# Kernel optimization log

Hardware: AMD Instinct MI355X
Metric: run time of the kernel (lower is better)

The kernel has to match this reference:

```python
import jax, jax.numpy as jnp
import numpy as np

B, T, C, H = 4, 4096, 1024, 64


def setup_inputs() -> dict:
    key = jax.random.key(0)
    k1, k2, k3, k4 = jax.random.split(key, 4)
    x = jax.random.normal(k1, (B, T, C), dtype=jnp.float32)
    # nn.Linear(C, H, bias=False) weights, stored as [C, H] so y = x @ W
    Wq = jax.random.normal(k2, (C, H), dtype=jnp.float32) * (C ** -0.5)
    Wk = jax.random.normal(k3, (C, H), dtype=jnp.float32) * (C ** -0.5)
    Wv = jax.random.normal(k4, (C, H), dtype=jnp.float32) * (C ** -0.5)
    return {"x": x, "Wq": Wq, "Wk": Wk, "Wv": Wv}


def reference(x, Wq, Wk, Wv):
    # x: (B,T,C) -> q,k,v: (B,T,H)
    q = jnp.einsum('btc,ch->bth', x, Wq)
    k = jnp.einsum('btc,ch->bth', x, Wk)
    v = jnp.einsum('btc,ch->bth', x, Wv)
    scale = q.shape[-1] ** -0.5
    # (B,T,T) attention scores with causal mask
    scores = jnp.einsum('bqh,bkh->bqk', q, k) * scale
    t = x.shape[1]
    causal = jnp.tril(jnp.ones((t, t), dtype=bool))
    scores = jnp.where(causal, scores, -jnp.inf)
    attn = jax.nn.softmax(scores, axis=-1)
    return jnp.einsum('bqk,bkh->bqh', attn, v)
```

## Files before the change

kernel.cpp:

```cpp
#include <hip/hip_runtime.h>

#define BATCH 4
#define SEQ   4096
#define CDIM  1024
#define HDIM  64

typedef __attribute__((ext_vector_type(8))) short bf16x8;
typedef __attribute__((ext_vector_type(4))) float f32x4;

#define WT_OFF 0
#define Q_OFF  (3 * HDIM * CDIM)
#define KF_OFF (Q_OFF + BATCH * SEQ * HDIM)
#define VF_OFF (KF_OFF + BATCH * SEQ * HDIM)

static __device__ __forceinline__ short f2bf(float f) {
  union { float f; unsigned u; } a; a.f = f;
  unsigned r = a.u + 0x7fffu + ((a.u >> 16) & 1u);
  return (short)(r >> 16);
}

static __device__ __forceinline__ bf16x8 ld8(const short* p) {
  return *(const bf16x8*)p;
}

__global__ void wcvt_kernel(const float* __restrict__ wq, const float* __restrict__ wk,
                            const float* __restrict__ wv, short* __restrict__ wt2) {
  int idx = blockIdx.x * 256 + threadIdx.x;
  int m = idx >> 16;
  int f = idx & 65535;
  int k0g = f >> 11, hc = (f >> 9) & 3, lr = (f >> 5) & 15, lg = (f >> 3) & 3, j = f & 7;
  int c = k0g * 32 + lg * 8 + j, h = hc * 16 + lr;
  const float* w = (m == 0) ? wq : (m == 1) ? wk : wv;
  wt2[((k0g * 12 + m * 4 + hc) * 64 + lr * 4 + lg) * 8 + j] = f2bf(w[c * 64 + h]);
}

__global__ __launch_bounds__(768, 6) void proj_kernel(const float* __restrict__ x,
                                                      const short* __restrict__ wt2,
                                                      short* __restrict__ ws) {
  __shared__ short xs2[2][32 * 256];
  __shared__ short k_lds[4][2][16][16];
  __shared__ short v_lds[4][2][16][16];

  int tid = threadIdx.x;
  int widx = tid >> 6, lane = tid & 63;
  int lr = lane & 15, lg = lane >> 4;
  int row0 = blockIdx.x * 32;
  int p = widx;
  int m = p >> 2, hcw = p & 3;

  int sr = tid >> 4, sci = tid & 15;
  const float* xsrc = x + (size_t)(row0 + sr) * CDIM + sci * 16;
  int sbase = sr * 512;
  int sxor = (sr & 7) << 4;

  int abase0 = lr * 512, abase1 = (16 + lr) * 512;
  int axor = (lr & 7) << 4;

  const short* bptr = wt2 + p * 512 + (lr * 4 + lg) * 8;

  f32x4 acc[2] = {};

#define PLOAD(RG, P) do {                                                    \
    _Pragma("unroll")                                                        \
    for (int q = 0; q < 4; ++q)                                              \
      RG[q] = *(const float4*)(xsrc + (P) * 256 + q * 4);                    \
  } while (0)

#define PSTORE(RG, BUF) do {                                                 \
    char* bc_ = (char*)&xs2[(BUF)][0];                                       \
    _Pragma("unroll")                                                        \
    for (int q = 0; q < 4; ++q) {                                            \
      uint2 u_;                                                              \
      u_.x = (unsigned)(unsigned short)f2bf(RG[q].x) |                       \
             ((unsigned)(unsigned short)f2bf(RG[q].y) << 16);                \
      u_.y = (unsigned)(unsigned short)f2bf(RG[q].z) |                       \
             ((unsigned)(unsigned short)f2bf(RG[q].w) << 16);                \
      *(uint2*)(bc_ + sbase + ((sci * 32 + q * 8) ^ sxor)) = u_;             \
    }                                                                        \
  } while (0)

#define PCOMPUTE(BUF, P) do {                                                \
    const char* bufc_ = (const char*)&xs2[(BUF)][0];                         \
    _Pragma("unroll")                                                        \
    for (int kk = 0; kk < 8; ++kk) {                                         \
      int co_ = (kk * 64 + lg * 16) ^ axor;                                  \
      bf16x8 af0_ = *(const bf16x8*)(bufc_ + abase0 + co_);                  \
      bf16x8 af1_ = *(const bf16x8*)(bufc_ + abase1 + co_);                  \
      bf16x8 bf_  = ld8(bptr + ((P) * 8 + kk) * 6144);                       \
      acc[0] = __builtin_amdgcn_mfma_f32_16x16x32_bf16(af0_, bf_, acc[0], 0, 0, 0); \
      acc[1] = __builtin_amdgcn_mfma_f32_16x16x32_bf16(af1_, bf_, acc[1], 0, 0, 0); \
    }                                                                        \
  } while (0)

  if (tid < 512) {
    float4 rg[4];
    PLOAD(rg, 0);
    PSTORE(rg, 0);
  }
  __syncthreads();
#pragma unroll
  for (int ph = 0; ph < 4; ++ph) {
    float4 rg[4];
    if (ph < 3 && tid < 512) PLOAD(rg, ph + 1);
    PCOMPUTE(ph & 1, ph);
    if (ph < 3) {
      if (tid < 512) PSTORE(rg, (ph + 1) & 1);
      __syncthreads();
    }
  }

  short* qs  = ws + Q_OFF;
  short* kfr = ws + KF_OFF;
  short* vfr = ws + VF_OFF;

  if (m == 0) {
#pragma unroll
    for (int rt = 0; rt < 2; ++rt) {
      int rbase = row0 + rt * 16;
#pragma unroll
      for (int reg = 0; reg < 4; ++reg)
        qs[(rbase + lg * 4 + reg) * 64 + hcw * 16 + lr] = f2bf(acc[rt][reg]);
    }
  } else if (m == 1) {
#pragma unroll
    for (int rt = 0; rt < 2; ++rt)
#pragma unroll
      for (int reg = 0; reg < 4; ++reg)
        k_lds[hcw][rt][lg * 4 + reg][lr] = f2bf(acc[rt][reg]);
    if (lane < 32) {
      int i0 = lane >> 1, f8 = (lane & 1) * 8;
#pragma unroll
      for (int rt = 0; rt < 2; ++rt) {
        int rbase = row0 + rt * 16;
        int b = rbase >> 12, tb = rbase & (SEQ - 1);
        int kb64 = tb >> 6, st = (tb >> 4) & 3;
        size_t kblk = ((((size_t)b * 64 + kb64) * 4 + st) * 2 + (hcw >> 1)) * 512;
        bf16x8 kv8 = *(const bf16x8*)(&k_lds[hcw][rt][i0][f8]);
        *(bf16x8*)(kfr + kblk + ((hcw & 1) * 2 + (f8 >> 3)) * 128 + i0 * 8) = kv8;
      }
    }
  } else {
#pragma unroll
    for (int rt = 0; rt < 2; ++rt)
#pragma unroll
      for (int reg = 0; reg < 4; ++reg)
        v_lds[hcw][rt][lr][lg * 4 + reg] = f2bf(acc[rt][reg]);
    if (lane < 32) {
      int i0 = lane >> 1, f8 = (lane & 1) * 8;
#pragma unroll
      for (int rt = 0; rt < 2; ++rt) {
        int rbase = row0 + rt * 16;
        int b = rbase >> 12, tb = rbase & (SEQ - 1);
        int kb64 = tb >> 6;
        size_t vblk = ((((size_t)b * 64 + kb64) * 2 + ((tb >> 5) & 1)) * 4 + hcw) * 512;
        bf16x8 vv8 = *(const bf16x8*)(&v_lds[hcw][rt][i0][f8]);
        *(bf16x8*)(vfr + vblk + (((tb & 16) + f8) >> 3) * 128 + i0 * 8) = vv8;
      }
    }
  }
}

__global__ __launch_bounds__(512, 4) void attn_kernel(const short* __restrict__ ws,
                                                      float* __restrict__ out) {
  __shared__ float p_o[8][4][4][64];
  __shared__ float p_l[8][4][64];
  __shared__ short plds[8][16][72];

  int widx = threadIdx.x >> 6, lane = threadIdx.x & 63;
  int lr = lane & 15, lg = lane >> 4;
  int g = blockIdx.x;

  const short* qs  = ws + Q_OFF;
  const short* kfr = ws + KF_OFF;
  const short* vfr = ws + VF_OFF;
  short* myp = &plds[widx][0][0];

  for (int tt = 0; tt < 2; ++tt) {
    int j = tt == 0 ? g : 1023 - g;
    int t16 = 255 - (j >> 2), b = j & 3;
    int qrow0 = b * SEQ + t16 * 16;
    int nkv = (t16 >> 2) + 1;

    bf16x8 qf0 = ld8(qs + (qrow0 + lr) * 64 + lg * 8);
    bf16x8 qf1 = ld8(qs + (qrow0 + lr) * 64 + 32 + lg * 8);
    const short* kb_b = kfr + (size_t)b * 64 * 4096 + lane * 8;
    const short* vb_b = vfr + (size_t)b * 64 * 4096 + lane * 8;

    f32x4 o[4] = {};
    float l_run[4] = {};

    if (tt) __syncthreads();

    bf16x8 kf[8];
    int kvb = widx;
    if (kvb < nkv) {
      const short* kb = kb_b + (size_t)kvb * 4096;
#pragma unroll
      for (int q8 = 0; q8 < 8; ++q8) kf[q8] = ld8(kb + q8 * 512);
    }

    for (; kvb < nkv; kvb += 8) {
      int kv0 = kvb * 64;

      f32x4 s[4] = {};
#pragma unroll
      for (int st = 0; st < 4; ++st) {
        s[st] = __builtin_amdgcn_mfma_f32_16x16x32_bf16(qf0, kf[st * 2],     s[st], 0, 0, 0);
        s[st] = __builtin_amdgcn_mfma_f32_16x16x32_bf16(qf1, kf[st * 2 + 1], s[st], 0, 0, 0);
      }

      bf16x8 vv[8];
      {
        const short* vb = vb_b + (size_t)kvb * 4096;
#pragma unroll
        for (int q8 = 0; q8 < 8; ++q8) vv[q8] = ld8(vb + q8 * 512);
      }
      int kvn = kvb + 8;
      if (kvn < nkv) {
        const short* kb = kb_b + (size_t)kvn * 4096;
#pragma unroll
        for (int q8 = 0; q8 < 8; ++q8) kf[q8] = ld8(kb + q8 * 512);
      }

      bool last = (kvb == nkv - 1);
#pragma unroll
      for (int reg = 0; reg < 4; ++reg) {
        int ig = t16 * 16 + lg * 4 + reg;
#pragma unroll
        for (int st = 0; st < 4; ++st) {
          float v = s[st][reg] * 0.125f;
          if (last && (kv0 + st * 16 + lr > ig)) v = -1e30f;
          float p = __expf(v);
          l_run[reg] += p;
          myp[(lg * 4 + reg) * 72 + st * 16 + lr] = f2bf(p);
        }
      }
      asm volatile("s_waitcnt lgkmcnt(0)" ::: "memory");
      bf16x8 pf0 = ld8(myp + lr * 72 + lg * 8);
      bf16x8 pf1 = ld8(myp + lr * 72 + 32 + lg * 8);

#pragma unroll
      for (int hc = 0; hc < 4; ++hc) {
        o[hc] = __builtin_amdgcn_mfma_f32_16x16x32_bf16(pf0, vv[hc],     o[hc], 0, 0, 0);
        o[hc] = __builtin_amdgcn_mfma_f32_16x16x32_bf16(pf1, vv[4 + hc], o[hc], 0, 0, 0);
      }
    }

#pragma unroll
    for (int reg = 0; reg < 4; ++reg) {
      float l = l_run[reg];
      l += __shfl_xor(l, 1);
      l += __shfl_xor(l, 2);
      l += __shfl_xor(l, 4);
      l += __shfl_xor(l, 8);
      l_run[reg] = l;
    }

#pragma unroll
    for (int hc = 0; hc < 4; ++hc)
#pragma unroll
      for (int reg = 0; reg < 4; ++reg)
        p_o[widx][hc][reg][lane] = o[hc][reg];
#pragma unroll
    for (int reg = 0; reg < 4; ++reg)
      p_l[widx][reg][lane] = l_run[reg];
    __syncthreads();

    if (widx < 4) {
      int reg = widx;
      float lsum = 0.f;
#pragma unroll
      for (int w = 0; w < 8; ++w) lsum += p_l[w][reg][lane];
      float inv = 1.0f / lsum;
#pragma unroll
      for (int hc = 0; hc < 4; ++hc) {
        float sv = 0.f;
#pragma unroll
        for (int w = 0; w < 8; ++w) sv += p_o[w][hc][reg][lane];
        out[(qrow0 + lg * 4 + reg) * 64 + hc * 16 + lr] = sv * inv;
      }
    }
  }
}

extern "C" void kernel_launch(void* const* d_in, const int* in_sizes, int n_in,
                              void* d_out, int out_size, void* d_ws, size_t ws_size,
                              hipStream_t stream) {
  const float* x  = (const float*)d_in[0];
  const float* wq = (const float*)d_in[1];
  const float* wk = (const float*)d_in[2];
  const float* wv = (const float*)d_in[3];
  short* ws = (short*)d_ws;
  float* out = (float*)d_out;

  wcvt_kernel<<<dim3(768), dim3(256), 0, stream>>>(wq, wk, wv, ws + WT_OFF);
  proj_kernel<<<dim3(512), dim3(768), 0, stream>>>(x, ws + WT_OFF, ws);
  attn_kernel<<<dim3(512), dim3(512), 0, stream>>>(ws, out);
}
```

Baseline: 60.04 us.

## Pre-convert x to bf16 in a separate pass and stage it via direct global-to-LDS loads

The weight-conversion kernel now also converts all of x from fp32 to bf16 into workspace, using packed bf16 convert instructions. The projection kernel then copies the bf16 x tiles straight into LDS with global_load_lds, with no register staging or in-kernel conversion. This is meant to cut VGPR use and conversion ALU work inside the projection kernel and to use asynchronous LDS fills. In exchange it adds a full extra pass over x: an fp32 read plus a bf16 write to workspace, then a bf16 re-read.

```diff
diff --git a/kernel.cpp b/kernel.cpp
--- a/kernel.cpp
+++ b/kernel.cpp
@@ -8,10 +8,11 @@
 typedef __attribute__((ext_vector_type(8))) short bf16x8;
 typedef __attribute__((ext_vector_type(4))) float f32x4;
 
-#define WT_OFF 0
-#define Q_OFF  (3 * HDIM * CDIM)
-#define KF_OFF (Q_OFF + BATCH * SEQ * HDIM)
-#define VF_OFF (KF_OFF + BATCH * SEQ * HDIM)
+#define WT_OFF  0
+#define Q_OFF   (3 * HDIM * CDIM)
+#define KF_OFF  (Q_OFF + BATCH * SEQ * HDIM)
+#define VF_OFF  (KF_OFF + BATCH * SEQ * HDIM)
+#define XBF_OFF (VF_OFF + BATCH * SEQ * HDIM)
 
 static __device__ __forceinline__ short f2bf(float f) {
   union { float f; unsigned u; } a; a.f = f;
@@ -19,25 +20,52 @@
   return (short)(r >> 16);
 }
 
+static __device__ __forceinline__ unsigned cvtpk(float lo, float hi) {
+  unsigned r;
+  asm("v_cvt_pk_bf16_f32 %0, %1, %2" : "=v"(r) : "v"(lo), "v"(hi));
+  return r;
+}
+
 static __device__ __forceinline__ bf16x8 ld8(const short* p) {
   return *(const bf16x8*)p;
 }
 
-__global__ void wcvt_kernel(const float* __restrict__ wq, const float* __restrict__ wk,
-                            const float* __restrict__ wv, short* __restrict__ wt2) {
-  int idx = blockIdx.x * 256 + threadIdx.x;
-  int m = idx >> 16;
-  int f = idx & 65535;
-  int k0g = f >> 11, hc = (f >> 9) & 3, lr = (f >> 5) & 15, lg = (f >> 3) & 3, j = f & 7;
-  int c = k0g * 32 + lg * 8 + j, h = hc * 16 + lr;
-  const float* w = (m == 0) ? wq : (m == 1) ? wk : wv;
-  wt2[((k0g * 12 + m * 4 + hc) * 64 + lr * 4 + lg) * 8 + j] = f2bf(w[c * 64 + h]);
-}
-
-__global__ __launch_bounds__(768, 6) void proj_kernel(const float* __restrict__ x,
+static __device__ __forceinline__ void gld_lds16(const short* g, short* l) {
+  __builtin_amdgcn_global_load_lds(
+      (const __attribute__((address_space(1))) void*)g,
+      (__attribute__((address_space(3))) void*)l, 16, 0, 0);
+}
+
+__global__ void cvt_kernel(const float* __restrict__ x,
+                           const float* __restrict__ wq, const float* __restrict__ wk,
+                           const float* __restrict__ wv, short* __restrict__ ws) {
+  int gb = blockIdx.x;
+  if (gb < 8192) {
+    int idx = gb * 256 + threadIdx.x;
+    const float* src = x + (size_t)idx * 8;
+    float4 f1 = *(const float4*)src;
+    float4 f2 = *(const float4*)(src + 4);
+    union { unsigned u[4]; bf16x8 v; } o;
+    o.u[0] = cvtpk(f1.x, f1.y);
+    o.u[1] = cvtpk(f1.z, f1.w);
+    o.u[2] = cvtpk(f2.x, f2.y);
+    o.u[3] = cvtpk(f2.z, f2.w);
+    *(bf16x8*)(ws + XBF_OFF + (size_t)idx * 8) = o.v;
+  } else {
+    int idx = (gb - 8192) * 256 + threadIdx.x;
+    int m = idx >> 16;
+    int f = idx & 65535;
+    int k0g = f >> 11, hc = (f >> 9) & 3, lr = (f >> 5) & 15, lg = (f >> 3) & 3, j = f & 7;
+    int c = k0g * 32 + lg * 8 + j, h = hc * 16 + lr;
+    const float* w = (m == 0) ? wq : (m == 1) ? wk : wv;
+    ws[WT_OFF + ((k0g * 12 + m * 4 + hc) * 64 + lr * 4 + lg) * 8 + j] = f2bf(w[c * 64 + h]);
+  }
+}
+
+__global__ __launch_bounds__(768, 6) void proj_kernel(const short* __restrict__ xbf,
                                                       const short* __restrict__ wt2,
                                                       short* __restrict__ ws) {
-  __shared__ short xs2[2][32 * 256];
+  __shared__ short xlds[2][32 * 256];
   __shared__ short k_lds[4][2][16][16];
   __shared__ short v_lds[4][2][16][16];
 
@@ -48,10 +76,21 @@
   int p = widx;
   int m = p >> 2, hcw = p & 3;
 
-  int sr = tid >> 4, sci = tid & 15;
-  const float* xsrc = x + (size_t)(row0 + sr) * CDIM + sci * 16;
-  int sbase = sr * 512;
-  int sxor = (sr & 7) << 4;
+  int srow2a = widx * 4;
+  int slrow0 = srow2a + (lane >> 5);
+  int slrow1 = srow2a + 2 + (lane >> 5);
+  int sck = (lane & 31) * 16;
+  int soff0 = sck ^ ((slrow0 & 7) << 4);
+  int soff1 = sck ^ ((slrow1 & 7) << 4);
+  const short* xsrc0 = xbf + (size_t)(row0 + slrow0) * 1024 + (soff0 >> 1);
+  const short* xsrc1 = xbf + (size_t)(row0 + slrow1) * 1024 + (soff1 >> 1);
+
+#define STAGE(BUF, PH) do {                                                  \
+    if (widx < 8) {                                                          \
+      gld_lds16(xsrc0 + (PH) * 256, &xlds[(BUF)][srow2a * 256]);             \
+      gld_lds16(xsrc1 + (PH) * 256, &xlds[(BUF)][(srow2a + 2) * 256]);       \
+    }                                                                        \
+  } while (0)
 
   int abase0 = lr * 512, abase1 = (16 + lr) * 512;
   int axor = (lr & 7) << 4;
@@ -60,53 +99,26 @@
 
   f32x4 acc[2] = {};
 
-#define PLOAD(RG, P) do {                                                    \
-    _Pragma("unroll")                                                        \
-    for (int q = 0; q < 4; ++q)                                              \
-      RG[q] = *(const float4*)(xsrc + (P) * 256 + q * 4);                    \
-  } while (0)
-
-#define PSTORE(RG, BUF) do {                                                 \
-    char* bc_ = (char*)&xs2[(BUF)][0];                                       \
-    _Pragma("unroll")                                                        \
-    for (int q = 0; q < 4; ++q) {                                            \
-      uint2 u_;                                                              \
-      u_.x = (unsigned)(unsigned short)f2bf(RG[q].x) |                       \
-             ((unsigned)(unsigned short)f2bf(RG[q].y) << 16);                \
-      u_.y = (unsigned)(unsigned short)f2bf(RG[q].z) |                       \
-             ((unsigned)(unsigned short)f2bf(RG[q].w) << 16);                \
-      *(uint2*)(bc_ + sbase + ((sci * 32 + q * 8) ^ sxor)) = u_;             \
-    }                                                                        \
-  } while (0)
-
-#define PCOMPUTE(BUF, P) do {                                                \
-    const char* bufc_ = (const char*)&xs2[(BUF)][0];                         \
+#define PCOMPUTE(BUF, PH) do {                                               \
+    const char* bufc_ = (const char*)&xlds[(BUF)][0];                        \
     _Pragma("unroll")                                                        \
     for (int kk = 0; kk < 8; ++kk) {                                         \
       int co_ = (kk * 64 + lg * 16) ^ axor;                                  \
       bf16x8 af0_ = *(const bf16x8*)(bufc_ + abase0 + co_);                  \
       bf16x8 af1_ = *(const bf16x8*)(bufc_ + abase1 + co_);                  \
-      bf16x8 bf_  = ld8(bptr + ((P) * 8 + kk) * 6144);                       \
+      bf16x8 bf_  = ld8(bptr + ((PH) * 8 + kk) * 6144);                      \
       acc[0] = __builtin_amdgcn_mfma_f32_16x16x32_bf16(af0_, bf_, acc[0], 0, 0, 0); \
       acc[1] = __builtin_amdgcn_mfma_f32_16x16x32_bf16(af1_, bf_, acc[1], 0, 0, 0); \
     }                                                                        \
   } while (0)
 
-  if (tid < 512) {
-    float4 rg[4];
-    PLOAD(rg, 0);
-    PSTORE(rg, 0);
-  }
+  STAGE(0, 0);
   __syncthreads();
 #pragma unroll
   for (int ph = 0; ph < 4; ++ph) {
-    float4 rg[4];
-    if (ph < 3 && tid < 512) PLOAD(rg, ph + 1);
+    if (ph < 3) STAGE((ph + 1) & 1, ph + 1);
     PCOMPUTE(ph & 1, ph);
-    if (ph < 3) {
-      if (tid < 512) PSTORE(rg, (ph + 1) & 1);
-      __syncthreads();
-    }
+    __syncthreads();
   }
 
   short* qs  = ws + Q_OFF;
@@ -293,7 +305,7 @@
   short* ws = (short*)d_ws;
   float* out = (float*)d_out;
 
-  wcvt_kernel<<<dim3(768), dim3(256), 0, stream>>>(wq, wk, wv, ws + WT_OFF);
-  proj_kernel<<<dim3(512), dim3(768), 0, stream>>>(x, ws + WT_OFF, ws);
+  cvt_kernel<<<dim3(8960), dim3(256), 0, stream>>>(x, wq, wk, wv, ws);
+  proj_kernel<<<dim3(512), dim3(768), 0, stream>>>(ws + XBF_OFF, ws + WT_OFF, ws);
   attn_kernel<<<dim3(512), dim3(512), 0, stream>>>(ws, out);
 }
```

Measured after the change: 64.71 us. +7.8%, slower.

## Double projection row tile to 64 and use packed bf16 conversion

Applied to the files above, without the earlier changes.

The QKV projection kernel now processes 64 rows per block instead of 32, halving the grid to 256 blocks. Each weight fragment loaded from global memory is reused across four MFMA row tiles instead of two. The fp32-to-bf16 staging uses the hardware v_cvt_pk_bf16_f32 instruction and writes 16-byte LDS stores instead of 8-byte ones. LDS use and register pressure grow and the launch bound drops to 3 blocks per CU, so a 256-block grid may leave some CUs idle.

```diff
diff --git a/kernel.cpp b/kernel.cpp
--- a/kernel.cpp
+++ b/kernel.cpp
@@ -8,15 +8,21 @@
 typedef __attribute__((ext_vector_type(8))) short bf16x8;
 typedef __attribute__((ext_vector_type(4))) float f32x4;
 
-#define WT_OFF 0
-#define Q_OFF  (3 * HDIM * CDIM)
-#define KF_OFF (Q_OFF + BATCH * SEQ * HDIM)
-#define VF_OFF (KF_OFF + BATCH * SEQ * HDIM)
+#define WT_OFF  0
+#define Q_OFF   (3 * HDIM * CDIM)
+#define KF_OFF  (Q_OFF + BATCH * SEQ * HDIM)
+#define VF_OFF  (KF_OFF + BATCH * SEQ * HDIM)
 
 static __device__ __forceinline__ short f2bf(float f) {
   union { float f; unsigned u; } a; a.f = f;
   unsigned r = a.u + 0x7fffu + ((a.u >> 16) & 1u);
   return (short)(r >> 16);
+}
+
+static __device__ __forceinline__ unsigned cvtpk(float lo, float hi) {
+  unsigned r;
+  asm("v_cvt_pk_bf16_f32 %0, %1, %2" : "=v"(r) : "v"(lo), "v"(hi));
+  return r;
 }
 
 static __device__ __forceinline__ bf16x8 ld8(const short* p) {
@@ -34,73 +40,73 @@
   wt2[((k0g * 12 + m * 4 + hc) * 64 + lr * 4 + lg) * 8 + j] = f2bf(w[c * 64 + h]);
 }
 
-__global__ __launch_bounds__(768, 6) void proj_kernel(const float* __restrict__ x,
+__global__ __launch_bounds__(768, 3) void proj_kernel(const float* __restrict__ x,
                                                       const short* __restrict__ wt2,
                                                       short* __restrict__ ws) {
-  __shared__ short xs2[2][32 * 256];
-  __shared__ short k_lds[4][2][16][16];
-  __shared__ short v_lds[4][2][16][16];
+  __shared__ short xph[2][64 * 256];
+  __shared__ short k_lds[4][4][16][16];
+  __shared__ short v_lds[4][4][16][16];
 
   int tid = threadIdx.x;
   int widx = tid >> 6, lane = tid & 63;
   int lr = lane & 15, lg = lane >> 4;
-  int row0 = blockIdx.x * 32;
+  int row0 = blockIdx.x * 64;
   int p = widx;
   int m = p >> 2, hcw = p & 3;
 
-  int sr = tid >> 4, sci = tid & 15;
-  const float* xsrc = x + (size_t)(row0 + sr) * CDIM + sci * 16;
+  int sr = tid >> 3, sc8 = tid & 7;
+  const float* xsrc = x + (size_t)(row0 + sr) * CDIM + sc8 * 32;
   int sbase = sr * 512;
   int sxor = (sr & 7) << 4;
 
-  int abase0 = lr * 512, abase1 = (16 + lr) * 512;
   int axor = (lr & 7) << 4;
 
   const short* bptr = wt2 + p * 512 + (lr * 4 + lg) * 8;
 
-  f32x4 acc[2] = {};
-
-#define PLOAD(RG, P) do {                                                    \
+  f32x4 acc[4] = {};
+
+#define PLOAD(RG, PH) do {                                                   \
     _Pragma("unroll")                                                        \
-    for (int q = 0; q < 4; ++q)                                              \
-      RG[q] = *(const float4*)(xsrc + (P) * 256 + q * 4);                    \
+    for (int q = 0; q < 8; ++q)                                              \
+      RG[q] = *(const float4*)(xsrc + (PH) * 256 + q * 4);                   \
   } while (0)
 
 #define PSTORE(RG, BUF) do {                                                 \
-    char* bc_ = (char*)&xs2[(BUF)][0];                                       \
+    char* bc_ = (char*)&xph[(BUF)][0];                                       \
     _Pragma("unroll")                                                        \
-    for (int q = 0; q < 4; ++q) {                                            \
-      uint2 u_;                                                              \
-      u_.x = (unsigned)(unsigned short)f2bf(RG[q].x) |                       \
-             ((unsigned)(unsigned short)f2bf(RG[q].y) << 16);                \
-      u_.y = (unsigned)(unsigned short)f2bf(RG[q].z) |                       \
-             ((unsigned)(unsigned short)f2bf(RG[q].w) << 16);                \
-      *(uint2*)(bc_ + sbase + ((sci * 32 + q * 8) ^ sxor)) = u_;             \
+    for (int d = 0; d < 4; ++d) {                                            \
+      union { unsigned u[4]; bf16x8 v; } o_;                                 \
+      o_.u[0] = cvtpk(RG[d * 2].x, RG[d * 2].y);                             \
+      o_.u[1] = cvtpk(RG[d * 2].z, RG[d * 2].w);                             \
+      o_.u[2] = cvtpk(RG[d * 2 + 1].x, RG[d * 2 + 1].y);                     \
+      o_.u[3] = cvtpk(RG[d * 2 + 1].z, RG[d * 2 + 1].w);                     \
+      *(bf16x8*)(bc_ + sbase + ((sc8 * 64 + d * 16) ^ sxor)) = o_.v;         \
     }                                                                        \
   } while (0)
 
-#define PCOMPUTE(BUF, P) do {                                                \
-    const char* bufc_ = (const char*)&xs2[(BUF)][0];                         \
+#define PCOMPUTE(BUF, PH) do {                                               \
+    const char* bufc_ = (const char*)&xph[(BUF)][0];                         \
     _Pragma("unroll")                                                        \
     for (int kk = 0; kk < 8; ++kk) {                                         \
       int co_ = (kk * 64 + lg * 16) ^ axor;                                  \
-      bf16x8 af0_ = *(const bf16x8*)(bufc_ + abase0 + co_);                  \
-      bf16x8 af1_ = *(const bf16x8*)(bufc_ + abase1 + co_);                  \
-      bf16x8 bf_  = ld8(bptr + ((P) * 8 + kk) * 6144);                       \
-      acc[0] = __builtin_amdgcn_mfma_f32_16x16x32_bf16(af0_, bf_, acc[0], 0, 0, 0); \
-      acc[1] = __builtin_amdgcn_mfma_f32_16x16x32_bf16(af1_, bf_, acc[1], 0, 0, 0); \
+      bf16x8 bf_ = ld8(bptr + ((PH) * 8 + kk) * 6144);                       \
+      _Pragma("unroll")                                                      \
+      for (int t = 0; t < 4; ++t) {                                          \
+        bf16x8 af_ = *(const bf16x8*)(bufc_ + (t * 16 + lr) * 512 + co_);    \
+        acc[t] = __builtin_amdgcn_mfma_f32_16x16x32_bf16(af_, bf_, acc[t], 0, 0, 0); \
+      }                                                                      \
     }                                                                        \
   } while (0)
 
   if (tid < 512) {
-    float4 rg[4];
+    float4 rg[8];
     PLOAD(rg, 0);
     PSTORE(rg, 0);
   }
   __syncthreads();
 #pragma unroll
   for (int ph = 0; ph < 4; ++ph) {
-    float4 rg[4];
+    float4 rg[8];
     if (ph < 3 && tid < 512) PLOAD(rg, ph + 1);
     PCOMPUTE(ph & 1, ph);
     if (ph < 3) {
@@ -115,7 +121,7 @@
 
   if (m == 0) {
 #pragma unroll
-    for (int rt = 0; rt < 2; ++rt) {
+    for (int rt = 0; rt < 4; ++rt) {
       int rbase = row0 + rt * 16;
 #pragma unroll
       for (int reg = 0; reg < 4; ++reg)
@@ -123,14 +129,14 @@
     }
   } else if (m == 1) {
 #pragma unroll
-    for (int rt = 0; rt < 2; ++rt)
+    for (int rt = 0; rt < 4; ++rt)
 #pragma unroll
       for (int reg = 0; reg < 4; ++reg)
         k_lds[hcw][rt][lg * 4 + reg][lr] = f2bf(acc[rt][reg]);
     if (lane < 32) {
       int i0 = lane >> 1, f8 = (lane & 1) * 8;
 #pragma unroll
-      for (int rt = 0; rt < 2; ++rt) {
+      for (int rt = 0; rt < 4; ++rt) {
         int rbase = row0 + rt * 16;
         int b = rbase >> 12, tb = rbase & (SEQ - 1);
         int kb64 = tb >> 6, st = (tb >> 4) & 3;
@@ -141,14 +147,14 @@
     }
   } else {
 #pragma unroll
-    for (int rt = 0; rt < 2; ++rt)
+    for (int rt = 0; rt < 4; ++rt)
 #pragma unroll
       for (int reg = 0; reg < 4; ++reg)
         v_lds[hcw][rt][lr][lg * 4 + reg] = f2bf(acc[rt][reg]);
     if (lane < 32) {
       int i0 = lane >> 1, f8 = (lane & 1) * 8;
 #pragma unroll
-      for (int rt = 0; rt < 2; ++rt) {
+      for (int rt = 0; rt < 4; ++rt) {
         int rbase = row0 + rt * 16;
         int b = rbase >> 12, tb = rbase & (SEQ - 1);
         int kb64 = tb >> 6;
@@ -270,13 +276,13 @@
       int reg = widx;
       float lsum = 0.f;
 #pragma unroll
-      for (int w = 0; w < 8; ++w) lsum += p_l[w][reg][lane];
+      for (int w2 = 0; w2 < 8; ++w2) lsum += p_l[w2][reg][lane];
       float inv = 1.0f / lsum;
 #pragma unroll
       for (int hc = 0; hc < 4; ++hc) {
         float sv = 0.f;
 #pragma unroll
-        for (int w = 0; w < 8; ++w) sv += p_o[w][hc][reg][lane];
+        for (int w2 = 0; w2 < 8; ++w2) sv += p_o[w2][hc][reg][lane];
         out[(qrow0 + lg * 4 + reg) * 64 + hc * 16 + lr] = sv * inv;
       }
     }
@@ -294,6 +300,6 @@
   float* out = (float*)d_out;
 
   wcvt_kernel<<<dim3(768), dim3(256), 0, stream>>>(wq, wk, wv, ws + WT_OFF);
-  proj_kernel<<<dim3(512), dim3(768), 0, stream>>>(x, ws + WT_OFF, ws);
+  proj_kernel<<<dim3(256), dim3(768), 0, stream>>>(x, ws + WT_OFF, ws);
   attn_kernel<<<dim3(512), dim3(512), 0, stream>>>(ws, out);
 }
```

Result: faster. 57.06 us (-5.0%).
